# Kernel optimization log

Measured on AMD Instinct MI355X. Metric: run time of the kernel, lower is better.

## Reference

```python
import jax, jax.numpy as jnp
import numpy as np

_SQRT2 = 1.4142135623730951

def _norm_cdf(z):
    return 0.5 * (1.0 + jax.scipy.special.erf(z / _SQRT2))

def _cv_squared(v):
    # torch.var is unbiased (ddof=1)
    return jnp.var(v, ddof=1) / (jnp.mean(v) ** 2 + 1e-10)

def setup_inputs() -> dict:
    key = jax.random.key(0)
    ks = jax.random.split(key, 6)
    B, Cin, Cout, H, W, E = 64, 32, 32, 64, 64, 16
    return {
        "x": jax.random.normal(ks[0], (B, Cin, H, W), jnp.float32),
        "noise": jax.random.normal(ks[1], (B, E), jnp.float32),
        "w_gate": jax.random.normal(ks[2], (Cin, E), jnp.float32) * 0.1,
        "w_noise": jax.random.normal(ks[3], (Cin, E), jnp.float32) * 0.1,
        "expert_w": jax.random.normal(ks[4], (E, Cout, Cin, 3, 3), jnp.float32) * 0.05,
        "expert_b": jax.random.normal(ks[5], (E, Cout), jnp.float32) * 0.05,
    }

def _forward(x, noise, w_gate, w_noise, expert_w, expert_b, k=4, loss_coef=0.01, noise_eps=0.01):
    B = x.shape[0]
    # gate features: adaptive avg pool to 1x1 then flatten -> [B, Cin]
    gate_x = x.mean(axis=(2, 3))
    clean = gate_x @ w_gate                      # [B, E]
    std = jax.nn.softplus(gate_x @ w_noise) + noise_eps
    noisy = clean + noise * std                  # noisy logits (training path)
    logits = jax.nn.softmax(noisy, axis=1)       # NOTE: original softmaxes before top-k
    top_logits, top_idx = jax.lax.top_k(logits, k + 1)
    top_k_logits = top_logits[:, :k]
    top_k_idx = top_idx[:, :k]
    top_k_gates = top_k_logits / (top_k_logits.sum(1, keepdims=True) + 1e-6)
    gates = jnp.zeros_like(logits).at[jnp.arange(B)[:, None], top_k_idx].set(top_k_gates)
    # _prob_in_top_k: thresholds come from the post-softmax top values,
    # compared against pre-softmax clean/noisy logits (faithful to source)
    thr_in = top_logits[:, k:k + 1]
    thr_out = top_logits[:, k - 1:k]
    prob = jnp.where(noisy > thr_in,
                     _norm_cdf((clean - thr_in) / std),
                     _norm_cdf((clean - thr_out) / std))
    load = prob.sum(0)
    importance = gates.sum(0)
    loss = (_cv_squared(importance) + _cv_squared(load)) * loss_coef
    # dispatch/combine: since gates are exactly zero for unselected experts,
    # sum_e gates[:,e] * expert_e(x) equals SparseDispatcher's gather-compute-scatter.
    def step(acc, xs):
        w, b, g = xs  # w [Co,Ci,3,3], b [Co], g [B]
        out = jax.lax.conv_general_dilated(x, w, (1, 1), [(1, 1), (1, 1)])
        out = out + b[None, :, None, None]
        return acc + g[:, None, None, None] * out, None
    y0 = jnp.zeros((B, expert_w.shape[1], x.shape[2], x.shape[3]), x.dtype)
    y, _ = jax.lax.scan(step, y0, (expert_w, expert_b, gates.T))
    return y, loss

def reference(x, noise, w_gate, w_noise, expert_w, expert_b):
    return _forward(x, noise, w_gate, w_noise, expert_w, expert_b)
```

## Files before the change

kernel.cpp:

```cpp
#include <hip/hip_runtime.h>
#include <math.h>

#define B 64
#define CIN 32
#define COUT 32
#define E 16
#define TOPK 4

typedef __attribute__((ext_vector_type(8))) short short8;
typedef __attribute__((ext_vector_type(4))) float f32x4;

__device__ __forceinline__ unsigned short f2bf(float f) {
    unsigned int u = __float_as_uint(f);
    u += 0x7fffu + ((u >> 16) & 1u);
    return (unsigned short)(u >> 16);
}

__device__ __forceinline__ int swz1024(int o) { return (o & 7) * 128 + (o >> 3); }

__device__ __forceinline__ int cswz(int wp, int c) {
    return c ^ (((wp >> 2) & 3) << 3);
}

__global__ void __launch_bounds__(256)
bandsum_kernel(const float* __restrict__ x, float* __restrict__ bandsum) {
    int blk = swz1024(blockIdx.x);
    int b = blk >> 4, band = blk & 15, h0 = band << 2;
    int t = threadIdx.x, wave = t >> 6, l = t & 63;
    const float4* x4 = reinterpret_cast<const float4*>(x);

    float racc[8];
    #pragma unroll
    for (int k = 0; k < 8; k++) {
        int c = k * 4 + wave;
        float4 v = x4[(((size_t)(b * 32 + c) * 64 + h0 + (l >> 4)) << 4) + (l & 15)];
        racc[k] = (v.x + v.y) + (v.z + v.w);
    }
    #pragma unroll
    for (int off = 1; off < 64; off <<= 1)
        #pragma unroll
        for (int k = 0; k < 8; k++) racc[k] += __shfl_xor(racc[k], off, 64);
    if (l == 0) {
        #pragma unroll
        for (int k = 0; k < 8; k++)
            bandsum[((size_t)b * 16 + band) * 32 + k * 4 + wave] = racc[k];
    }
}

__global__ void __launch_bounds__(256)
gate_combine(const float* __restrict__ bandsum,
             const float* __restrict__ noise,
             const float* __restrict__ w_gate,
             const float* __restrict__ w_noise,
             const float* __restrict__ expert_w,
             const float* __restrict__ expert_b,
             unsigned short* __restrict__ cwb,
             float* __restrict__ cbias,
             float* __restrict__ probw,
             float* __restrict__ gimpw) {
    int blk = swz1024(blockIdx.x);
    int b = blk >> 4, s = blk & 15;
    int t = threadIdx.x;

    __shared__ float elds[16 * 576];
    __shared__ float gx[32];
    __shared__ float s_tv[TOPK + 1], s_g[TOPK];
    __shared__ int   s_gi[TOPK];

    const float4* ew4 = reinterpret_cast<const float4*>(expert_w);
    float4 stg[9];
    #pragma unroll
    for (int k = 0; k < 9; k++) {
        int j = k * 256 + t;
        int e = j / 144, off = j - e * 144;
        stg[k] = ew4[(size_t)e * 2304 + s * 144 + off];
    }

    if (t < 32) {
        const float* bp = bandsum + (size_t)b * 512 + t;
        float acc = 0.f;
        #pragma unroll
        for (int j = 0; j < 16; j++) acc += bp[j * 32];
        gx[t] = acc * (1.f / 4096.f);
    }

    #pragma unroll
    for (int k = 0; k < 9; k++) {
        int j = k * 256 + t;
        *reinterpret_cast<float4*>(&elds[j * 4]) = stg[k];
    }

    if (t < 16) {
        float s1 = 0.f, s2 = 0.f;
        #pragma unroll
        for (int c = 0; c < CIN; c++) {
            float g = gx[c];
            s1 += g * w_gate[c * E + t];
            s2 += g * w_noise[c * E + t];
        }
        float sp   = fmaxf(s2, 0.f) + log1pf(expf(-fabsf(s2)));
        float stdv = sp + 0.01f;
        float noisy = s1 + noise[b * E + t] * stdv;

        float m = noisy;
        #pragma unroll
        for (int off = 1; off < 16; off <<= 1) m = fmaxf(m, __shfl_xor(m, off, 16));
        float ex = expf(noisy - m);
        float den = ex;
        #pragma unroll
        for (int off = 1; off < 16; off <<= 1) den += __shfl_xor(den, off, 16);
        float lg = ex / den;

        int rank = 0;
        #pragma unroll
        for (int j = 0; j < E; j++) {
            float u = __shfl(lg, j, 16);
            rank += (u > lg) || (u == lg && j < t);
        }
        if (rank <= TOPK) s_tv[rank] = lg;
        if (rank <  TOPK) s_gi[rank] = t;
        float s4 = s_tv[0] + s_tv[1] + s_tv[2] + s_tv[3] + 1e-6f;
        if (rank < TOPK) s_g[rank] = lg / s4;

        if (s == 0) {
            gimpw[b * E + t] = (rank < TOPK) ? lg / s4 : 0.f;
            const float INV_SQRT2 = 0.70710678118654752f;
            float thr_in = s_tv[TOPK], thr_out = s_tv[TOPK - 1];
            float thr = (noisy > thr_in) ? thr_in : thr_out;
            float z = (s1 - thr) / stdv;
            probw[b * E + t] = 0.5f * (1.f + erff(z * INV_SQRT2));
        }
    }
    __syncthreads();

    float g0 = s_g[0], g1 = s_g[1], g2 = s_g[2], g3 = s_g[3];
    int   i0 = s_gi[0], i1 = s_gi[1], i2 = s_gi[2], i3 = s_gi[3];
    for (int local = t; local < 576; local += 256) {
        int tap = local >> 6, ccl = local & 63;
        int rdl = ccl * 9 + tap;
        float v = g0 * elds[i0 * 576 + rdl] + g1 * elds[i1 * 576 + rdl]
                + g2 * elds[i2 * 576 + rdl] + g3 * elds[i3 * 576 + rdl];
        cwb[(size_t)b * 9216 + tap * 1024 + s * 64 + ccl] = f2bf(v);
    }
    if (s == 0 && t < COUT) {
        cbias[b * COUT + t] = g0 * expert_b[i0 * 32 + t] + g1 * expert_b[i1 * 32 + t]
                            + g2 * expert_b[i2 * 32 + t] + g3 * expert_b[i3 * 32 + t];
    }
}

__global__ void __launch_bounds__(256)
conv_mfma(const float* __restrict__ x,
          const unsigned short* __restrict__ cwb,
          const float* __restrict__ cbias,
          const float* __restrict__ probw,
          const float* __restrict__ gimpw,
          float* __restrict__ y,
          float* __restrict__ loss_out) {
    int blk = swz1024(blockIdx.x);
    int b = blk >> 4, band = blk & 15, h0 = band << 2;
    int t = threadIdx.x, wave = t >> 6, l = t & 63;
    int ln = l & 15, lk = l >> 4;

    __shared__ unsigned short sx[6 * 66 * 32];

    const unsigned short* wbase = cwb + (size_t)b * 9216;
    short8 afrag[2][9];
    #pragma unroll
    for (int tap = 0; tap < 9; tap++)
        #pragma unroll
        for (int ch = 0; ch < 2; ch++)
            afrag[ch][tap] = *reinterpret_cast<const short8*>(
                wbase + tap * 1024 + (ch * 16 + ln) * 32 + lk * 8);
    float bias0[4], bias1[4];
    #pragma unroll
    for (int r = 0; r < 4; r++) {
        bias0[r] = cbias[b * COUT + lk * 4 + r];
        bias1[r] = cbias[b * COUT + 16 + lk * 4 + r];
    }

    const float4* x4 = reinterpret_cast<const float4*>(x);
    #pragma unroll
    for (int k = 0; k < 12; k++) {
        int i = k * 256 + t;
        int rr = i >> 9, c = (i >> 4) & 31, w4 = i & 15;
        int gr = h0 - 1 + rr;
        float4 v = {0.f, 0.f, 0.f, 0.f};
        if ((unsigned)gr < 64u)
            v = x4[(((size_t)(b * 32 + c) * 64 + gr) << 4) + w4];
        float vv[4] = {v.x, v.y, v.z, v.w};
        #pragma unroll
        for (int j = 0; j < 4; j++) {
            int wp = 1 + w4 * 4 + j;
            sx[(rr * 66 + wp) * 32 + cswz(wp, c)] = f2bf(vv[j]);
        }
    }
    for (int i = t; i < 384; i += 256) {
        int rr = i >> 6, rem = i & 63, side = rem >> 5, c = rem & 31;
        sx[(rr * 66 + side * 65) * 32 + c] = 0;
    }
    __syncthreads();

    int h = h0 + wave;
    for (int tile = 0; tile < 4; tile++) {
        int w0 = tile * 16;
        f32x4 acc0 = {0.f, 0.f, 0.f, 0.f};
        f32x4 acc1 = {0.f, 0.f, 0.f, 0.f};
        #pragma unroll
        for (int kh = 0; kh < 3; kh++) {
            int rr = wave + kh;
            #pragma unroll
            for (int kw = 0; kw < 3; kw++) {
                int wp = w0 + ln + kw;
                short8 bfrag = *reinterpret_cast<const short8*>(
                    &sx[(rr * 66 + wp) * 32 + cswz(wp, lk * 8)]);
                acc0 = __builtin_amdgcn_mfma_f32_16x16x32_bf16(afrag[0][kh * 3 + kw], bfrag, acc0, 0, 0, 0);
                acc1 = __builtin_amdgcn_mfma_f32_16x16x32_bf16(afrag[1][kh * 3 + kw], bfrag, acc1, 0, 0, 0);
            }
        }
        #pragma unroll
        for (int r = 0; r < 4; r++) {
            y[((size_t)(b * COUT + lk * 4 + r) * 64 + h) * 64 + w0 + ln]      = acc0[r] + bias0[r];
            y[((size_t)(b * COUT + 16 + lk * 4 + r) * 64 + h) * 64 + w0 + ln] = acc1[r] + bias1[r];
        }
    }

    if (blk == 0) {
        __shared__ float s_lv[32];
        if (t < 32) {
            const float* src = (t < 16) ? gimpw : probw;
            int e = t & 15;
            float s = 0.f;
            for (int bb = 0; bb < B; bb++) s += src[bb * E + e];
            s_lv[t] = s;
        }
        __syncthreads();
        if (t == 0) {
            float loss = 0.f;
            for (int pass = 0; pass < 2; pass++) {
                const float* v = s_lv + pass * 16;
                float mean = 0.f;
                for (int e = 0; e < E; e++) mean += v[e];
                mean *= (1.f / E);
                float var = 0.f;
                for (int e = 0; e < E; e++) { float d = v[e] - mean; var += d * d; }
                var *= (1.f / (E - 1));
                loss += var / (mean * mean + 1e-10f);
            }
            loss_out[0] = loss * 0.01f;
        }
    }
}

extern "C" void kernel_launch(void* const* d_in, const int* in_sizes, int n_in,
                              void* d_out, int out_size, void* d_ws, size_t ws_size,
                              hipStream_t stream) {
    const float* x        = (const float*)d_in[0];
    const float* noise    = (const float*)d_in[1];
    const float* w_gate   = (const float*)d_in[2];
    const float* w_noise  = (const float*)d_in[3];
    const float* expert_w = (const float*)d_in[4];
    const float* expert_b = (const float*)d_in[5];

    float* y    = (float*)d_out;
    float* loss = y + (size_t)B * COUT * 64 * 64;

    char* ws = (char*)d_ws;
    float*          bands  = (float*)(ws);
    float*          probw  = (float*)(ws + 131072);
    float*          gimpw  = (float*)(ws + 135168);
    float*          cbias  = (float*)(ws + 139264);
    unsigned short* cwb    = (unsigned short*)(ws + 147456);

    bandsum_kernel<<<B * 16, 256, 0, stream>>>(x, bands);
    gate_combine<<<B * 16, 256, 0, stream>>>(bands, noise, w_gate, w_noise,
                                             expert_w, expert_b, cwb, cbias,
                                             probw, gimpw);
    conv_mfma<<<B * 16, 256, 0, stream>>>(x, cwb, cbias, probw, gimpw, y, loss);
}
```

Baseline: 33.80 us.

## Fuse bandsum and gate/combine kernels via per-batch last-block arrival counter

Merges the band-sum reduction and the gating/weight-combine kernel into one launch. Each block writes its band partial sums, then atomically bumps a per-batch arrival counter, and only the last block for each batch computes the gate, top-k, prob/importance and the full 9216-element combined bf16 weights. This removes one kernel launch and the redundant per-block staging of expert weights into LDS, but adds a memset launch and serializes the combine work onto 64 blocks, each doing 36 strided gathered loads per thread.

```diff
diff --git a/kernel.cpp b/kernel.cpp
--- a/kernel.cpp
+++ b/kernel.cpp
@@ -23,73 +23,62 @@
 }
 
 __global__ void __launch_bounds__(256)
-bandsum_kernel(const float* __restrict__ x, float* __restrict__ bandsum) {
-    int blk = swz1024(blockIdx.x);
-    int b = blk >> 4, band = blk & 15, h0 = band << 2;
-    int t = threadIdx.x, wave = t >> 6, l = t & 63;
-    const float4* x4 = reinterpret_cast<const float4*>(x);
-
-    float racc[8];
-    #pragma unroll
-    for (int k = 0; k < 8; k++) {
-        int c = k * 4 + wave;
-        float4 v = x4[(((size_t)(b * 32 + c) * 64 + h0 + (l >> 4)) << 4) + (l & 15)];
-        racc[k] = (v.x + v.y) + (v.z + v.w);
-    }
-    #pragma unroll
-    for (int off = 1; off < 64; off <<= 1)
-        #pragma unroll
-        for (int k = 0; k < 8; k++) racc[k] += __shfl_xor(racc[k], off, 64);
-    if (l == 0) {
-        #pragma unroll
-        for (int k = 0; k < 8; k++)
-            bandsum[((size_t)b * 16 + band) * 32 + k * 4 + wave] = racc[k];
-    }
-}
-
-__global__ void __launch_bounds__(256)
-gate_combine(const float* __restrict__ bandsum,
+bandsum_gate(const float* __restrict__ x,
              const float* __restrict__ noise,
              const float* __restrict__ w_gate,
              const float* __restrict__ w_noise,
              const float* __restrict__ expert_w,
              const float* __restrict__ expert_b,
+             float* __restrict__ bandsum,
+             int* __restrict__ arrival,
              unsigned short* __restrict__ cwb,
              float* __restrict__ cbias,
              float* __restrict__ probw,
              float* __restrict__ gimpw) {
     int blk = swz1024(blockIdx.x);
-    int b = blk >> 4, s = blk & 15;
-    int t = threadIdx.x;
-
-    __shared__ float elds[16 * 576];
+    int b = blk >> 4, band = blk & 15, h0 = band << 2;
+    int t = threadIdx.x, wave = t >> 6, l = t & 63;
+    const float4* x4 = reinterpret_cast<const float4*>(x);
+
+    {
+        float racc[8];
+        #pragma unroll
+        for (int k = 0; k < 8; k++) {
+            int c = k * 4 + wave;
+            float4 v = x4[(((size_t)(b * 32 + c) * 64 + h0 + (l >> 4)) << 4) + (l & 15)];
+            racc[k] = (v.x + v.y) + (v.z + v.w);
+        }
+        #pragma unroll
+        for (int off = 1; off < 64; off <<= 1)
+            #pragma unroll
+            for (int k = 0; k < 8; k++) racc[k] += __shfl_xor(racc[k], off, 64);
+        if (l == 0) {
+            #pragma unroll
+            for (int k = 0; k < 8; k++)
+                bandsum[((size_t)b * 16 + band) * 32 + k * 4 + wave] = racc[k];
+        }
+    }
+
+    __syncthreads();
+    __shared__ int s_win;
+    if (t == 0) {
+        __threadfence();
+        s_win = atomicAdd(&arrival[b], 1);
+    }
+    __syncthreads();
+    if (s_win != 15) return;
+
     __shared__ float gx[32];
     __shared__ float s_tv[TOPK + 1], s_g[TOPK];
     __shared__ int   s_gi[TOPK];
 
-    const float4* ew4 = reinterpret_cast<const float4*>(expert_w);
-    float4 stg[9];
-    #pragma unroll
-    for (int k = 0; k < 9; k++) {
-        int j = k * 256 + t;
-        int e = j / 144, off = j - e * 144;
-        stg[k] = ew4[(size_t)e * 2304 + s * 144 + off];
-    }
-
     if (t < 32) {
-        const float* bp = bandsum + (size_t)b * 512 + t;
+        const volatile float* bp = bandsum + (size_t)b * 512 + t;
         float acc = 0.f;
         #pragma unroll
         for (int j = 0; j < 16; j++) acc += bp[j * 32];
         gx[t] = acc * (1.f / 4096.f);
     }
-
-    #pragma unroll
-    for (int k = 0; k < 9; k++) {
-        int j = k * 256 + t;
-        *reinterpret_cast<float4*>(&elds[j * 4]) = stg[k];
-    }
-
     if (t < 16) {
         float s1 = 0.f, s2 = 0.f;
         #pragma unroll
@@ -122,27 +111,30 @@
         float s4 = s_tv[0] + s_tv[1] + s_tv[2] + s_tv[3] + 1e-6f;
         if (rank < TOPK) s_g[rank] = lg / s4;
 
-        if (s == 0) {
-            gimpw[b * E + t] = (rank < TOPK) ? lg / s4 : 0.f;
-            const float INV_SQRT2 = 0.70710678118654752f;
-            float thr_in = s_tv[TOPK], thr_out = s_tv[TOPK - 1];
-            float thr = (noisy > thr_in) ? thr_in : thr_out;
-            float z = (s1 - thr) / stdv;
-            probw[b * E + t] = 0.5f * (1.f + erff(z * INV_SQRT2));
-        }
+        gimpw[b * E + t] = (rank < TOPK) ? lg / s4 : 0.f;
+        const float INV_SQRT2 = 0.70710678118654752f;
+        float thr_in = s_tv[TOPK], thr_out = s_tv[TOPK - 1];
+        float thr = (noisy > thr_in) ? thr_in : thr_out;
+        float z = (s1 - thr) / stdv;
+        probw[b * E + t] = 0.5f * (1.f + erff(z * INV_SQRT2));
     }
     __syncthreads();
 
     float g0 = s_g[0], g1 = s_g[1], g2 = s_g[2], g3 = s_g[3];
     int   i0 = s_gi[0], i1 = s_gi[1], i2 = s_gi[2], i3 = s_gi[3];
-    for (int local = t; local < 576; local += 256) {
-        int tap = local >> 6, ccl = local & 63;
-        int rdl = ccl * 9 + tap;
-        float v = g0 * elds[i0 * 576 + rdl] + g1 * elds[i1 * 576 + rdl]
-                + g2 * elds[i2 * 576 + rdl] + g3 * elds[i3 * 576 + rdl];
-        cwb[(size_t)b * 9216 + tap * 1024 + s * 64 + ccl] = f2bf(v);
-    }
-    if (s == 0 && t < COUT) {
+    const float* e0 = expert_w + i0 * 9216;
+    const float* e1 = expert_w + i1 * 9216;
+    const float* e2 = expert_w + i2 * 9216;
+    const float* e3 = expert_w + i3 * 9216;
+    #pragma unroll
+    for (int k = 0; k < 36; k++) {
+        int i = k * 256 + t;
+        int tap = i >> 10, cc = i & 1023;
+        int rd = cc * 9 + tap;
+        float s = g0 * e0[rd] + g1 * e1[rd] + g2 * e2[rd] + g3 * e3[rd];
+        cwb[(size_t)b * 9216 + i] = f2bf(s);
+    }
+    if (t < COUT) {
         cbias[b * COUT + t] = g0 * expert_b[i0 * 32 + t] + g1 * expert_b[i1 * 32 + t]
                             + g2 * expert_b[i2 * 32 + t] + g3 * expert_b[i3 * 32 + t];
     }
@@ -265,15 +257,16 @@
     float* loss = y + (size_t)B * COUT * 64 * 64;
 
     char* ws = (char*)d_ws;
-    float*          bands  = (float*)(ws);
-    float*          probw  = (float*)(ws + 131072);
-    float*          gimpw  = (float*)(ws + 135168);
-    float*          cbias  = (float*)(ws + 139264);
-    unsigned short* cwb    = (unsigned short*)(ws + 147456);
-
-    bandsum_kernel<<<B * 16, 256, 0, stream>>>(x, bands);
-    gate_combine<<<B * 16, 256, 0, stream>>>(bands, noise, w_gate, w_noise,
-                                             expert_w, expert_b, cwb, cbias,
-                                             probw, gimpw);
+    float*          bands   = (float*)(ws);
+    float*          probw   = (float*)(ws + 131072);
+    float*          gimpw   = (float*)(ws + 135168);
+    float*          cbias   = (float*)(ws + 139264);
+    unsigned short* cwb     = (unsigned short*)(ws + 147456);
+    int*            arrival = (int*)(ws + 1327104);
+
+    hipMemsetAsync(arrival, 0, B * sizeof(int), stream);
+    bandsum_gate<<<B * 16, 256, 0, stream>>>(x, noise, w_gate, w_noise,
+                                             expert_w, expert_b, bands, arrival,
+                                             cwb, cbias, probw, gimpw);
     conv_mfma<<<B * 16, 256, 0, stream>>>(x, cwb, cbias, probw, gimpw, y, loss);
 }
```

Result: slower. 91.84 us (+171.7%).
